# Kernel tuning notes

Measured on AMD Instinct MI355X. Metric: run time of the kernel, lower is better.

The kernel has to match this reference:

```python
import jax, jax.numpy as jnp
import numpy as np

D_MODEL = 1024
D_INNER = 2048   # expand * d_model
D_STATE = 16
D_CONV = 4
DT_RANK = 64     # ceil(d_model / 16)
BATCH = 2
SEQLEN = 4096


def setup_inputs() -> dict:
    key = jax.random.key(0)
    ks = jax.random.split(key, 9)
    g = lambda k, shape, scale: jax.random.normal(k, shape, dtype=jnp.float32) * scale
    hidden_states = g(ks[0], (BATCH, SEQLEN, D_MODEL), 1.0)
    W_in = g(ks[1], (2 * D_INNER, D_MODEL), D_MODEL ** -0.5)
    conv_w = g(ks[2], (D_INNER, D_CONV), D_CONV ** -0.5)
    conv_b = g(ks[3], (D_INNER,), 0.02)
    x_proj_w = g(ks[4], (DT_RANK + 2 * D_STATE, D_INNER), D_INNER ** -0.5)
    dt_w = g(ks[5], (D_INNER, DT_RANK), DT_RANK ** -0.5)
    # dt bias init as in Mamba: inverse softplus of dt ~ U[log(1e-3), log(1e-1)]
    dt = jnp.exp(jax.random.uniform(ks[6], (D_INNER,), dtype=jnp.float32)
                 * (np.log(0.1) - np.log(0.001)) + np.log(0.001))
    dt = jnp.clip(dt, 1e-4, None)
    dt_b = dt + jnp.log(-jnp.expm1(-dt))
    # A_log init: log of [1..d_state] repeated per channel
    A_log = jnp.log(jnp.tile(jnp.arange(1, D_STATE + 1, dtype=jnp.float32), (D_INNER, 1)))
    D = jnp.ones((D_INNER,), dtype=jnp.float32)
    W_out = g(ks[7], (D_MODEL, D_INNER), D_INNER ** -0.5)
    return dict(hidden_states=hidden_states, W_in=W_in, conv_w=conv_w, conv_b=conv_b,
                x_proj_w=x_proj_w, dt_w=dt_w, dt_b=dt_b, A_log=A_log, D=D, W_out=W_out)


def reference(hidden_states, W_in, conv_w, conv_b, x_proj_w, dt_w, dt_b, A_log, D, W_out):
    B, L, _ = hidden_states.shape
    # in_proj + transpose -> (B, 2*Din, L)
    xz = jnp.einsum('bld,ed->bel', hidden_states, W_in)
    # nanotron (tp=1) splits via view(B, d_inner, 2, L): interleaved channels
    xz = xz.reshape(B, D_INNER, 2, L)
    x, z = xz[:, :, 0, :], xz[:, :, 1, :]          # (B, Din, L)
    # causal depthwise conv1d (pad left d_conv-1) + SiLU
    xc = jax.lax.conv_general_dilated(
        x, conv_w[:, None, :], window_strides=(1,), padding=[(D_CONV - 1, 0)],
        dimension_numbers=('NCH', 'OIH', 'NCH'), feature_group_count=D_INNER)
    x = jax.nn.silu(xc + conv_b[None, :, None])     # (B, Din, L)
    # x_proj -> dt, B, C
    x_dbl = jnp.einsum('bdl,ed->ble', x, x_proj_w)  # (B, L, dt_rank+2N)
    dt, Bm, Cm = jnp.split(x_dbl, [DT_RANK, DT_RANK + D_STATE], axis=-1)
    delta = jnp.einsum('blr,dr->bdl', dt, dt_w)     # (B, Din, L)
    delta = jax.nn.softplus(delta + dt_b[None, :, None])
    A = -jnp.exp(A_log)                             # (Din, N)
    # selective scan over time
    xs = (jnp.transpose(delta, (2, 0, 1)),          # (L, B, Din)
          jnp.transpose(x, (2, 0, 1)),              # (L, B, Din)
          jnp.transpose(Bm, (1, 0, 2)),             # (L, B, N)
          jnp.transpose(Cm, (1, 0, 2)))             # (L, B, N)

    def step(s, inp):
        d_t, x_t, B_t, C_t = inp
        s = s * jnp.exp(d_t[:, :, None] * A[None]) + (d_t * x_t)[:, :, None] * B_t[:, None, :]
        y_t = jnp.einsum('bdn,bn->bd', s, C_t)
        return s, y_t

    s0 = jnp.zeros((B, D_INNER, D_STATE), dtype=hidden_states.dtype)
    _, ys = jax.lax.scan(step, s0, xs)              # ys: (L, B, Din)
    y = jnp.transpose(ys, (1, 2, 0))                # (B, Din, L)
    y = y + D[None, :, None] * x
    y = y * jax.nn.silu(z)
    out = jnp.einsum('bdl,md->blm', y, W_out)       # (B, L, d_model)
    return out
```

## Files before the change

### kernel.cpp

```cpp
#include <hip/hip_runtime.h>
#include <hip/hip_bf16.h>

#define D_MODEL 1024
#define D_INNER 2048
#define D_STATE 16
#define DT_RANK 64
#define BATCH 2
#define SEQLEN 4096
#define BL (BATCH * SEQLEN)
#define NPROJ (DT_RANK + 2 * D_STATE)
#define CH 64
#define NCH (SEQLEN / CH)

typedef __attribute__((ext_vector_type(8))) short bf16x8;
typedef __attribute__((ext_vector_type(4))) float f32x4;
struct S4 { short x, y, z, w; };

__device__ __forceinline__ float sigmoidf_(float v) {
    return 1.0f / (1.0f + __expf(-v));
}

__device__ __forceinline__ unsigned short bf16_rne(float f) {
    unsigned u = __float_as_uint(f);
    unsigned r = u + 0x7FFFu + ((u >> 16) & 1u);
    return (unsigned short)(r >> 16);
}

__device__ __forceinline__ float bf2f(short s) {
    return __uint_as_float(((unsigned)(unsigned short)s) << 16);
}

__global__ __launch_bounds__(256)
void cvt_split(const float* __restrict__ in, short* __restrict__ hi,
               short* __restrict__ lo, int n4) {
    const int i = blockIdx.x * 256 + threadIdx.x;
    if (i >= n4) return;
    const float4 v = reinterpret_cast<const float4*>(in)[i];
    const float f[4] = {v.x, v.y, v.z, v.w};
    S4 h, l;
    short hb[4], lb[4];
#pragma unroll
    for (int j = 0; j < 4; ++j) {
        const unsigned short hh = bf16_rne(f[j]);
        const float hf = __uint_as_float((unsigned)hh << 16);
        hb[j] = (short)hh;
        lb[j] = (short)bf16_rne(f[j] - hf);
    }
    h.x = hb[0]; h.y = hb[1]; h.z = hb[2]; h.w = hb[3];
    l.x = lb[0]; l.y = lb[1]; l.z = lb[2]; l.w = lb[3];
    *reinterpret_cast<S4*>(hi + (size_t)i * 4) = h;
    *reinterpret_cast<S4*>(lo + (size_t)i * 4) = l;
}

template <int EPI>
__global__ __launch_bounds__(256)
void gemm_bf16x3(const short* __restrict__ Ahi, const short* __restrict__ Alo,
                 const short* __restrict__ Bhi, const short* __restrict__ Blo,
                 float* __restrict__ C, int K, int lda, int ldb, int ldc,
                 const float* __restrict__ bias) {
    __shared__ short sA[2][128][32];
    __shared__ short sB[2][128][32];
    const int t = threadIdx.x;
    const int w = t >> 6, l = t & 63;

    const int nwg = gridDim.x * gridDim.y;
    int bid = blockIdx.y * gridDim.x + blockIdx.x;
    if ((nwg & 7) == 0) bid = (bid & 7) * (nwg >> 3) + (bid >> 3);
    const int m0 = (bid / gridDim.x) * 128, n0 = (bid % gridDim.x) * 128;
    const int wr = w >> 1, wc = w & 1;

    const short* gsrc;
    short* sdst;
    int ld, tile0;
    if (w == 0)      { gsrc = Ahi; sdst = &sA[0][0][0]; tile0 = m0; ld = lda; }
    else if (w == 1) { gsrc = Alo; sdst = &sA[1][0][0]; tile0 = m0; ld = lda; }
    else if (w == 2) { gsrc = Bhi; sdst = &sB[0][0][0]; tile0 = n0; ld = ldb; }
    else             { gsrc = Blo; sdst = &sB[1][0][0]; tile0 = n0; ld = ldb; }
    const int kc_src = ((l & 3) ^ ((l >> 3) & 3)) << 3;
    const size_t grow = (size_t)(tile0 + (l >> 2)) * ld + kc_src;

    f32x4 acc[4][4] = {};
    const int frow = l & 15;
    const int kb = (((l >> 4) ^ ((frow >> 1) & 3)) << 3);

    for (int k0 = 0; k0 < K; k0 += 32) {
        __syncthreads();
#pragma unroll
        for (int i = 0; i < 8; ++i) {
            const short* g = gsrc + grow + (size_t)(i << 4) * ld + k0;
            __builtin_amdgcn_global_load_lds(
                (const __attribute__((address_space(1))) void*)g,
                (__attribute__((address_space(3))) void*)(sdst + (i << 9)),
                16, 0, 0);
        }
        __syncthreads();

        bf16x8 a[2][4], b[2][4];
#pragma unroll
        for (int f = 0; f < 4; ++f) {
            a[0][f] = *reinterpret_cast<const bf16x8*>(&sA[0][wr * 64 + f * 16 + frow][kb]);
            a[1][f] = *reinterpret_cast<const bf16x8*>(&sA[1][wr * 64 + f * 16 + frow][kb]);
            b[0][f] = *reinterpret_cast<const bf16x8*>(&sB[0][wc * 64 + f * 16 + frow][kb]);
            b[1][f] = *reinterpret_cast<const bf16x8*>(&sB[1][wc * 64 + f * 16 + frow][kb]);
        }
#pragma unroll
        for (int fi = 0; fi < 4; ++fi)
#pragma unroll
            for (int fj = 0; fj < 4; ++fj) {
                acc[fi][fj] = __builtin_amdgcn_mfma_f32_16x16x32_bf16(
                    a[0][fi], b[0][fj], acc[fi][fj], 0, 0, 0);
                acc[fi][fj] = __builtin_amdgcn_mfma_f32_16x16x32_bf16(
                    a[1][fi], b[0][fj], acc[fi][fj], 0, 0, 0);
                acc[fi][fj] = __builtin_amdgcn_mfma_f32_16x16x32_bf16(
                    a[0][fi], b[1][fj], acc[fi][fj], 0, 0, 0);
            }
    }

    const int crow = (l >> 4) << 2;
    const int ccol = l & 15;
#pragma unroll
    for (int fi = 0; fi < 4; ++fi)
#pragma unroll
        for (int fj = 0; fj < 4; ++fj) {
            const int n = n0 + wc * 64 + fj * 16 + ccol;
#pragma unroll
            for (int r = 0; r < 4; ++r) {
                float v = acc[fi][fj][r];
                if (EPI == 1) {
                    v += bias[n];
                    v = fmaxf(v, 0.f) + log1pf(__expf(-fabsf(v)));
                }
                C[(size_t)(m0 + wr * 64 + fi * 16 + crow + r) * ldc + n] = v;
            }
        }
}

__global__ __launch_bounds__(256)
void gemm96(const short* __restrict__ Xhi, const short* __restrict__ Xlo,
            const short* __restrict__ Whi, const short* __restrict__ Wlo,
            float* __restrict__ C, short* __restrict__ dthi,
            short* __restrict__ dtlo) {
    const int t = threadIdx.x;
    const int w = t >> 6, l = t & 63;
    const int m0 = blockIdx.x * 32;
    const int rfrag = (w >> 1) * 16;
    const int cbase = (w & 1) * 48;
    const int lrow = l & 15;
    const int koff0 = (l >> 4) << 3;
    f32x4 acc[3] = {};
    const size_t arow = (size_t)(m0 + rfrag + lrow) * D_INNER;
#pragma unroll 2
    for (int k0 = 0; k0 < D_INNER; k0 += 32) {
        const int ko = k0 + koff0;
        const bf16x8 ah = *reinterpret_cast<const bf16x8*>(Xhi + arow + ko);
        const bf16x8 al = *reinterpret_cast<const bf16x8*>(Xlo + arow + ko);
#pragma unroll
        for (int jj = 0; jj < 3; ++jj) {
            const size_t brow = (size_t)(cbase + jj * 16 + lrow) * D_INNER + ko;
            const bf16x8 bh = *reinterpret_cast<const bf16x8*>(Whi + brow);
            const bf16x8 bl = *reinterpret_cast<const bf16x8*>(Wlo + brow);
            acc[jj] = __builtin_amdgcn_mfma_f32_16x16x32_bf16(ah, bh, acc[jj], 0, 0, 0);
            acc[jj] = __builtin_amdgcn_mfma_f32_16x16x32_bf16(al, bh, acc[jj], 0, 0, 0);
            acc[jj] = __builtin_amdgcn_mfma_f32_16x16x32_bf16(ah, bl, acc[jj], 0, 0, 0);
        }
    }
    const int crow = (l >> 4) << 2;
#pragma unroll
    for (int jj = 0; jj < 3; ++jj) {
        const int col = cbase + jj * 16 + lrow;
#pragma unroll
        for (int r = 0; r < 4; ++r) {
            const int m = m0 + rfrag + crow + r;
            const float v = acc[jj][r];
            C[(size_t)m * NPROJ + col] = v;
            if (col < DT_RANK) {
                const unsigned short hh = bf16_rne(v);
                dthi[(size_t)m * DT_RANK + col] = (short)hh;
                dtlo[(size_t)m * DT_RANK + col] =
                    (short)bf16_rne(v - __uint_as_float((unsigned)hh << 16));
            }
        }
    }
}

__global__ __launch_bounds__(256)
void conv_silu_k(const float* __restrict__ xr, const float* __restrict__ cw,
                 const float* __restrict__ cb, short* __restrict__ xchi,
                 short* __restrict__ xclo) {
    const int idx = blockIdx.x * 256 + threadIdx.x;
    const int d = idx & (D_INNER - 1);
    const int bl = idx >> 11;
    const int l = bl & (SEQLEN - 1);
    const float4 w4 = *reinterpret_cast<const float4*>(cw + (size_t)d * 4);
    const float wj[4] = {w4.x, w4.y, w4.z, w4.w};
    float acc = cb[d];
#pragma unroll
    for (int j = 0; j < 4; ++j) {
        const int ll = l - 3 + j;
        if (ll >= 0)
            acc += xr[(size_t)(bl - 3 + j) * D_INNER + d] * wj[j];
    }
    const float v = acc * sigmoidf_(acc);
    const unsigned short hh = bf16_rne(v);
    xchi[idx] = (short)hh;
    xclo[idx] = (short)bf16_rne(v - __uint_as_float((unsigned)hh << 16));
}

__global__ __launch_bounds__(256)
void scan1(const float* __restrict__ delta, const short* __restrict__ xchi,
           const short* __restrict__ xclo, const float* __restrict__ dtbc,
           const float* __restrict__ A_log, float* __restrict__ sum_delta,
           float* __restrict__ S_end) {
    const int d = blockIdx.x * 256 + threadIdx.x;
    const int b = blockIdx.y;
    const int c = blockIdx.z;
    __shared__ float bc[CH][32];
    for (int i = threadIdx.x; i < CH * 32; i += 256) {
        const int row = i >> 5, col = i & 31;
        bc[row][col] = dtbc[(size_t)(b * SEQLEN + c * CH + row) * NPROJ + DT_RANK + col];
    }
    __syncthreads();
    float A[16];
#pragma unroll
    for (int n = 0; n < 16; ++n) A[n] = -__expf(A_log[(size_t)d * 16 + n]);
    float s[16] = {0.f};
    float sd = 0.f;
    const size_t base = ((size_t)b * SEQLEN + (size_t)c * CH) * D_INNER + d;
    for (int li = 0; li < CH; ++li) {
        const size_t o = base + (size_t)li * D_INNER;
        const float dl = delta[o];
        const float xv = bf2f(xchi[o]) + bf2f(xclo[o]);
        sd += dl;
        const float dx = dl * xv;
#pragma unroll
        for (int n = 0; n < 16; ++n) {
            const float a = __expf(dl * A[n]);
            s[n] = fmaf(s[n], a, dx * bc[li][n]);
        }
    }
    sum_delta[((size_t)c * BATCH + b) * D_INNER + d] = sd;
#pragma unroll
    for (int n = 0; n < 16; ++n)
        S_end[(((size_t)c * BATCH + b) * 16 + n) * D_INNER + d] = s[n];
}

__global__ __launch_bounds__(256)
void scan2(const float* __restrict__ sum_delta, float* __restrict__ S,
           const float* __restrict__ A_log) {
    const int idx = blockIdx.x * 256 + threadIdx.x;
    const int d = idx & (D_INNER - 1);
    const int n = (idx >> 11) & 15;
    const int b = idx >> 15;
    const float A = -__expf(A_log[(size_t)d * 16 + n]);
    float carry = 0.f;
    for (int c = 0; c < NCH; ++c) {
        const float sd = sum_delta[((size_t)c * BATCH + b) * D_INNER + d];
        const size_t o = (((size_t)c * BATCH + b) * 16 + n) * D_INNER + d;
        const float se = S[o];
        S[o] = carry;
        carry = fmaf(carry, __expf(sd * A), se);
    }
}

__global__ __launch_bounds__(256)
void scan3(const float* __restrict__ delta, short* __restrict__ xchi,
           short* __restrict__ xclo, const float* __restrict__ z,
           const float* __restrict__ dtbc, const float* __restrict__ A_log,
           const float* __restrict__ S_init, const float* __restrict__ Dp) {
    const int d = blockIdx.x * 256 + threadIdx.x;
    const int b = blockIdx.y;
    const int c = blockIdx.z;
    __shared__ float bc[CH][32];
    for (int i = threadIdx.x; i < CH * 32; i += 256) {
        const int row = i >> 5, col = i & 31;
        bc[row][col] = dtbc[(size_t)(b * SEQLEN + c * CH + row) * NPROJ + DT_RANK + col];
    }
    __syncthreads();
    float A[16];
#pragma unroll
    for (int n = 0; n < 16; ++n) A[n] = -__expf(A_log[(size_t)d * 16 + n]);
    float s[16];
#pragma unroll
    for (int n = 0; n < 16; ++n)
        s[n] = S_init[(((size_t)c * BATCH + b) * 16 + n) * D_INNER + d];
    const float Dv = Dp[d];
    const size_t base = ((size_t)b * SEQLEN + (size_t)c * CH) * D_INNER + d;
    for (int li = 0; li < CH; ++li) {
        const size_t o = base + (size_t)li * D_INNER;
        const float dl = delta[o];
        const float xv = bf2f(xchi[o]) + bf2f(xclo[o]);
        const float dx = dl * xv;
        float y = 0.f;
#pragma unroll
        for (int n = 0; n < 16; ++n) {
            const float a = __expf(dl * A[n]);
            s[n] = fmaf(s[n], a, dx * bc[li][n]);
            y = fmaf(s[n], bc[li][16 + n], y);
        }
        const float zv = z[o];
        const float yv = (y + Dv * xv) * (zv * sigmoidf_(zv));
        const unsigned short hh = bf16_rne(yv);
        xchi[o] = (short)hh;
        xclo[o] = (short)bf16_rne(yv - __uint_as_float((unsigned)hh << 16));
    }
}

extern "C" void kernel_launch(void* const* d_in, const int* in_sizes, int n_in,
                              void* d_out, int out_size, void* d_ws, size_t ws_size,
                              hipStream_t stream) {
    const float* hidden   = (const float*)d_in[0];
    const float* W_in     = (const float*)d_in[1];
    const float* conv_w   = (const float*)d_in[2];
    const float* conv_b   = (const float*)d_in[3];
    const float* x_proj_w = (const float*)d_in[4];
    const float* dt_w     = (const float*)d_in[5];
    const float* dt_b     = (const float*)d_in[6];
    const float* A_log    = (const float*)d_in[7];
    const float* Dp       = (const float*)d_in[8];
    const float* W_out    = (const float*)d_in[9];
    float* out = (float*)d_out;

    float* ws    = (float*)d_ws;
    float* xbuf  = ws;
    float* zbuf  = xbuf + (size_t)BL * D_INNER;
    float* xcreg = zbuf + (size_t)BL * D_INNER;
    float* dtbc  = xcreg + (size_t)BL * D_INNER;
    float* sumd  = dtbc + (size_t)BL * NPROJ;
    float* Send  = sumd + (size_t)NCH * BATCH * D_INNER;

    short* xpwhi = (short*)(Send + (size_t)NCH * BATCH * 16 * D_INNER);
    short* xpwlo = xpwhi + (size_t)NPROJ * D_INNER;
    short* dtwhi = xpwlo + (size_t)NPROJ * D_INNER;
    short* dtwlo = dtwhi + (size_t)D_INNER * DT_RANK;
    short* dthi  = dtwlo + (size_t)D_INNER * DT_RANK;
    short* dtlo  = dthi + (size_t)BL * DT_RANK;

    short* hxhi  = (short*)xcreg;
    short* hxlo  = hxhi + (size_t)BL * D_MODEL;
    short* winhi = hxlo + (size_t)BL * D_MODEL;
    short* winlo = winhi + (size_t)2 * D_INNER * D_MODEL;

    const dim3 thr(256);

    cvt_split<<<dim3(BL * D_MODEL / 1024), thr, 0, stream>>>(hidden, hxhi, hxlo, BL * D_MODEL / 4);
    cvt_split<<<dim3(2 * D_INNER * D_MODEL / 1024), thr, 0, stream>>>(W_in, winhi, winlo, 2 * D_INNER * D_MODEL / 4);
    cvt_split<<<dim3(NPROJ * D_INNER / 1024), thr, 0, stream>>>(x_proj_w, xpwhi, xpwlo, NPROJ * D_INNER / 4);
    cvt_split<<<dim3(D_INNER * DT_RANK / 1024), thr, 0, stream>>>(dt_w, dtwhi, dtwlo, D_INNER * DT_RANK / 4);

    gemm_bf16x3<0><<<dim3(D_INNER / 128, BL / 128), thr, 0, stream>>>(
        hxhi, hxlo, winhi, winlo, xbuf, D_MODEL, D_MODEL, 2 * D_MODEL, D_INNER, nullptr);
    gemm_bf16x3<0><<<dim3(D_INNER / 128, BL / 128), thr, 0, stream>>>(
        hxhi, hxlo, winhi + D_MODEL, winlo + D_MODEL, zbuf, D_MODEL, D_MODEL, 2 * D_MODEL, D_INNER, nullptr);

    short* xchi = (short*)xcreg;
    short* xclo = xchi + (size_t)BL * D_INNER;
    conv_silu_k<<<dim3(BL * D_INNER / 256), thr, 0, stream>>>(xbuf, conv_w, conv_b, xchi, xclo);

    gemm96<<<dim3(BL / 32), thr, 0, stream>>>(xchi, xclo, xpwhi, xpwlo, dtbc, dthi, dtlo);

    gemm_bf16x3<1><<<dim3(D_INNER / 128, BL / 128), thr, 0, stream>>>(
        dthi, dtlo, dtwhi, dtwlo, xbuf, DT_RANK, DT_RANK, DT_RANK, D_INNER, dt_b);

    scan1<<<dim3(D_INNER / 256, BATCH, NCH), thr, 0, stream>>>(
        xbuf, xchi, xclo, dtbc, A_log, sumd, Send);
    scan2<<<dim3(BATCH * 16 * D_INNER / 256), thr, 0, stream>>>(sumd, Send, A_log);
    scan3<<<dim3(D_INNER / 256, BATCH, NCH), thr, 0, stream>>>(
        xbuf, xchi, xclo, zbuf, dtbc, A_log, Send, Dp);

    short* wohi = (short*)zbuf;
    short* wolo = wohi + (size_t)D_MODEL * D_INNER;
    cvt_split<<<dim3(D_MODEL * D_INNER / 1024), thr, 0, stream>>>(W_out, wohi, wolo, D_MODEL * D_INNER / 4);

    gemm_bf16x3<0><<<dim3(D_MODEL / 128, BL / 128), thr, 0, stream>>>(
        xchi, xclo, wohi, wolo, out, D_INNER, D_INNER, D_INNER, D_MODEL, nullptr);
}
```

Before: 762.9 us.

## Double-buffer LDS tiles in bf16x3 GEMM to overlap global loads with MFMA

Doubles the shared-memory tiles and restructures the K loop so the next K-slice is fetched with global_load_lds while MFMAs run on the current slice. Explicit vmcnt waits and s_barrier calls replace the two __syncthreads per iteration. This hides global-to-LDS latency in the GEMMs, at the cost of twice the LDS per block (64KB), which may lower occupancy.

```diff
diff --git a/kernel.cpp b/kernel.cpp
--- a/kernel.cpp
+++ b/kernel.cpp
@@ -58,8 +58,8 @@
                  const short* __restrict__ Bhi, const short* __restrict__ Blo,
                  float* __restrict__ C, int K, int lda, int ldb, int ldc,
                  const float* __restrict__ bias) {
-    __shared__ short sA[2][128][32];
-    __shared__ short sB[2][128][32];
+    __shared__ short sA[2][2][128][32];
+    __shared__ short sB[2][2][128][32];
     const int t = threadIdx.x;
     const int w = t >> 6, l = t & 63;
 
@@ -70,12 +70,13 @@
     const int wr = w >> 1, wc = w & 1;
 
     const short* gsrc;
-    short* sdst;
+    short* sd0;
+    short* sd1;
     int ld, tile0;
-    if (w == 0)      { gsrc = Ahi; sdst = &sA[0][0][0]; tile0 = m0; ld = lda; }
-    else if (w == 1) { gsrc = Alo; sdst = &sA[1][0][0]; tile0 = m0; ld = lda; }
-    else if (w == 2) { gsrc = Bhi; sdst = &sB[0][0][0]; tile0 = n0; ld = ldb; }
-    else             { gsrc = Blo; sdst = &sB[1][0][0]; tile0 = n0; ld = ldb; }
+    if (w == 0)      { gsrc = Ahi; sd0 = &sA[0][0][0][0]; sd1 = &sA[1][0][0][0]; tile0 = m0; ld = lda; }
+    else if (w == 1) { gsrc = Alo; sd0 = &sA[0][1][0][0]; sd1 = &sA[1][1][0][0]; tile0 = m0; ld = lda; }
+    else if (w == 2) { gsrc = Bhi; sd0 = &sB[0][0][0][0]; sd1 = &sB[1][0][0][0]; tile0 = n0; ld = ldb; }
+    else             { gsrc = Blo; sd0 = &sB[0][1][0][0]; sd1 = &sB[1][1][0][0]; tile0 = n0; ld = ldb; }
     const int kc_src = ((l & 3) ^ ((l >> 3) & 3)) << 3;
     const size_t grow = (size_t)(tile0 + (l >> 2)) * ld + kc_src;
 
@@ -83,8 +84,7 @@
     const int frow = l & 15;
     const int kb = (((l >> 4) ^ ((frow >> 1) & 3)) << 3);
 
-    for (int k0 = 0; k0 < K; k0 += 32) {
-        __syncthreads();
+    auto STAGE = [&](short* sdst, int k0) {
 #pragma unroll
         for (int i = 0; i < 8; ++i) {
             const short* g = gsrc + grow + (size_t)(i << 4) * ld + k0;
@@ -93,15 +93,16 @@
                 (__attribute__((address_space(3))) void*)(sdst + (i << 9)),
                 16, 0, 0);
         }
-        __syncthreads();
-
+    };
+
+    auto COMPUTE = [&](int cur) {
         bf16x8 a[2][4], b[2][4];
 #pragma unroll
         for (int f = 0; f < 4; ++f) {
-            a[0][f] = *reinterpret_cast<const bf16x8*>(&sA[0][wr * 64 + f * 16 + frow][kb]);
-            a[1][f] = *reinterpret_cast<const bf16x8*>(&sA[1][wr * 64 + f * 16 + frow][kb]);
-            b[0][f] = *reinterpret_cast<const bf16x8*>(&sB[0][wc * 64 + f * 16 + frow][kb]);
-            b[1][f] = *reinterpret_cast<const bf16x8*>(&sB[1][wc * 64 + f * 16 + frow][kb]);
+            a[0][f] = *reinterpret_cast<const bf16x8*>(&sA[cur][0][wr * 64 + f * 16 + frow][kb]);
+            a[1][f] = *reinterpret_cast<const bf16x8*>(&sA[cur][1][wr * 64 + f * 16 + frow][kb]);
+            b[0][f] = *reinterpret_cast<const bf16x8*>(&sB[cur][0][wc * 64 + f * 16 + frow][kb]);
+            b[1][f] = *reinterpret_cast<const bf16x8*>(&sB[cur][1][wc * 64 + f * 16 + frow][kb]);
         }
 #pragma unroll
         for (int fi = 0; fi < 4; ++fi)
@@ -114,6 +115,26 @@
                 acc[fi][fj] = __builtin_amdgcn_mfma_f32_16x16x32_bf16(
                     a[0][fi], b[1][fj], acc[fi][fj], 0, 0, 0);
             }
+    };
+
+    const int NT = K >> 5;
+    STAGE(sd0, 0);
+    for (int tt = 0; tt < NT - 1; ++tt) {
+        const int cur = tt & 1;
+        STAGE(cur ? sd0 : sd1, (tt + 1) << 5);
+        __builtin_amdgcn_sched_barrier(0);
+        asm volatile("s_waitcnt vmcnt(8)" ::: "memory");
+        __builtin_amdgcn_s_barrier();
+        COMPUTE(cur);
+        __builtin_amdgcn_sched_barrier(0);
+        __builtin_amdgcn_s_barrier();
+    }
+    {
+        const int cur = (NT - 1) & 1;
+        __builtin_amdgcn_sched_barrier(0);
+        asm volatile("s_waitcnt vmcnt(0)" ::: "memory");
+        __builtin_amdgcn_s_barrier();
+        COMPUTE(cur);
     }
 
     const int crow = (l >> 4) << 2;
```

Result: faster. 709.4 us (-7.0%).

## Switch split GEMMs to fp16 two-term MFMA with fused x/z pipelined GEMM

Applied to the files above, without the earlier changes.

The three-term bf16 split (hi*hi + lo*hi + hi*lo) is replaced by an fp16 two-term split: only the activation keeps a hi/lo pair and the weight is a single fp16 value. The aim is to cut the MFMA count and the weight conversion and load traffic. The GEMM kernel moves to 256x128 tiles with 512 threads and a triple-buffered global_load_lds pipeline using explicit vmcnt waits. The x and z in_proj GEMMs are fused into one launch that splits the interleaved output columns in the epilogue. Delta and z are now stored as fp16 to halve scan traffic, at some risk to accuracy and fp16 range.

```diff
diff --git a/kernel.cpp b/kernel.cpp
--- a/kernel.cpp
+++ b/kernel.cpp
@@ -12,27 +12,39 @@
 #define CH 64
 #define NCH (SEQLEN / CH)
 
-typedef __attribute__((ext_vector_type(8))) short bf16x8;
+typedef __attribute__((ext_vector_type(8))) _Float16 f16x8;
 typedef __attribute__((ext_vector_type(4))) float f32x4;
 struct S4 { short x, y, z, w; };
 
 __device__ __forceinline__ float sigmoidf_(float v) {
     return 1.0f / (1.0f + __expf(-v));
 }
-
-__device__ __forceinline__ unsigned short bf16_rne(float f) {
-    unsigned u = __float_as_uint(f);
-    unsigned r = u + 0x7FFFu + ((u >> 16) & 1u);
-    return (unsigned short)(r >> 16);
-}
-
-__device__ __forceinline__ float bf2f(short s) {
-    return __uint_as_float(((unsigned)(unsigned short)s) << 16);
-}
-
-__global__ __launch_bounds__(256)
-void cvt_split(const float* __restrict__ in, short* __restrict__ hi,
-               short* __restrict__ lo, int n4) {
+__device__ __forceinline__ short f2h(float f) {
+    _Float16 h = (_Float16)f;
+    return __builtin_bit_cast(short, h);
+}
+__device__ __forceinline__ float h2f(short s) {
+    return (float)__builtin_bit_cast(_Float16, s);
+}
+
+#define GLOAD(gptr, dptr)                                              \
+    __builtin_amdgcn_global_load_lds(                                  \
+        (const __attribute__((address_space(1))) void*)(gptr),         \
+        (__attribute__((address_space(3))) void*)(dptr), 16, 0, 0)
+
+__global__ __launch_bounds__(256)
+void cvt_h(const float* __restrict__ in, short* __restrict__ out, int n4) {
+    const int i = blockIdx.x * 256 + threadIdx.x;
+    if (i >= n4) return;
+    const float4 v = reinterpret_cast<const float4*>(in)[i];
+    S4 o;
+    o.x = f2h(v.x); o.y = f2h(v.y); o.z = f2h(v.z); o.w = f2h(v.w);
+    *reinterpret_cast<S4*>(out + (size_t)i * 4) = o;
+}
+
+__global__ __launch_bounds__(256)
+void cvt_split_h(const float* __restrict__ in, short* __restrict__ hi,
+                 short* __restrict__ lo, int n4) {
     const int i = blockIdx.x * 256 + threadIdx.x;
     if (i >= n4) return;
     const float4 v = reinterpret_cast<const float4*>(in)[i];
@@ -41,10 +53,8 @@
     short hb[4], lb[4];
 #pragma unroll
     for (int j = 0; j < 4; ++j) {
-        const unsigned short hh = bf16_rne(f[j]);
-        const float hf = __uint_as_float((unsigned)hh << 16);
-        hb[j] = (short)hh;
-        lb[j] = (short)bf16_rne(f[j] - hf);
+        hb[j] = f2h(f[j]);
+        lb[j] = f2h(f[j] - h2f(hb[j]));
     }
     h.x = hb[0]; h.y = hb[1]; h.z = hb[2]; h.w = hb[3];
     l.x = lb[0]; l.y = lb[1]; l.z = lb[2]; l.w = lb[3];
@@ -53,67 +63,75 @@
 }
 
 template <int EPI>
-__global__ __launch_bounds__(256)
-void gemm_bf16x3(const short* __restrict__ Ahi, const short* __restrict__ Alo,
-                 const short* __restrict__ Bhi, const short* __restrict__ Blo,
-                 float* __restrict__ C, int K, int lda, int ldb, int ldc,
-                 const float* __restrict__ bias) {
-    __shared__ short sA[2][128][32];
-    __shared__ short sB[2][128][32];
+__global__ __launch_bounds__(512)
+void gemm_f16x2(const short* __restrict__ Ahi, const short* __restrict__ Alo,
+                const short* __restrict__ B, void* C0v, void* C1v,
+                int K, int lda, int ldb, int ldc,
+                const float* __restrict__ bias) {
+    extern __shared__ short smem[];
     const int t = threadIdx.x;
     const int w = t >> 6, l = t & 63;
 
     const int nwg = gridDim.x * gridDim.y;
     int bid = blockIdx.y * gridDim.x + blockIdx.x;
-    if ((nwg & 7) == 0) bid = (bid & 7) * (nwg >> 3) + (bid >> 3);
-    const int m0 = (bid / gridDim.x) * 128, n0 = (bid % gridDim.x) * 128;
+    bid = (bid & 7) * (nwg >> 3) + (bid >> 3);
+    const int m0 = (bid / gridDim.x) * 256, n0 = (bid % gridDim.x) * 128;
     const int wr = w >> 1, wc = w & 1;
 
-    const short* gsrc;
-    short* sdst;
-    int ld, tile0;
-    if (w == 0)      { gsrc = Ahi; sdst = &sA[0][0][0]; tile0 = m0; ld = lda; }
-    else if (w == 1) { gsrc = Alo; sdst = &sA[1][0][0]; tile0 = m0; ld = lda; }
-    else if (w == 2) { gsrc = Bhi; sdst = &sB[0][0][0]; tile0 = n0; ld = ldb; }
-    else             { gsrc = Blo; sdst = &sB[1][0][0]; tile0 = n0; ld = ldb; }
+    const int r4 = l >> 2;
     const int kc_src = ((l & 3) ^ ((l >> 3) & 3)) << 3;
-    const size_t grow = (size_t)(tile0 + (l >> 2)) * ld + kc_src;
-
-    f32x4 acc[4][4] = {};
     const int frow = l & 15;
     const int kb = (((l >> 4) ^ ((frow >> 1) & 3)) << 3);
 
-    for (int k0 = 0; k0 < K; k0 += 32) {
-        __syncthreads();
-#pragma unroll
-        for (int i = 0; i < 8; ++i) {
-            const short* g = gsrc + grow + (size_t)(i << 4) * ld + k0;
-            __builtin_amdgcn_global_load_lds(
-                (const __attribute__((address_space(1))) void*)g,
-                (__attribute__((address_space(3))) void*)(sdst + (i << 9)),
-                16, 0, 0);
-        }
-        __syncthreads();
-
-        bf16x8 a[2][4], b[2][4];
+    f32x4 acc[4][4] = {};
+
+    auto STAGE = [&](int buf, int k0) {
+        short* bb = smem + buf * 20480;
+        const int s0 = 2 * w, s1 = 2 * w + 1;
+        GLOAD(Ahi + (size_t)(m0 + s0 * 16 + r4) * lda + k0 + kc_src, bb + s0 * 512);
+        GLOAD(Ahi + (size_t)(m0 + s1 * 16 + r4) * lda + k0 + kc_src, bb + s1 * 512);
+        GLOAD(Alo + (size_t)(m0 + s0 * 16 + r4) * lda + k0 + kc_src, bb + 8192 + s0 * 512);
+        GLOAD(Alo + (size_t)(m0 + s1 * 16 + r4) * lda + k0 + kc_src, bb + 8192 + s1 * 512);
+        GLOAD(B + (size_t)(n0 + w * 16 + r4) * ldb + k0 + kc_src, bb + 16384 + w * 512);
+    };
+
+    auto COMPUTE = [&](int buf) {
+        const short* bb = smem + buf * 20480;
+        f16x8 ah[4], al[4], bv[4];
 #pragma unroll
         for (int f = 0; f < 4; ++f) {
-            a[0][f] = *reinterpret_cast<const bf16x8*>(&sA[0][wr * 64 + f * 16 + frow][kb]);
-            a[1][f] = *reinterpret_cast<const bf16x8*>(&sA[1][wr * 64 + f * 16 + frow][kb]);
-            b[0][f] = *reinterpret_cast<const bf16x8*>(&sB[0][wc * 64 + f * 16 + frow][kb]);
-            b[1][f] = *reinterpret_cast<const bf16x8*>(&sB[1][wc * 64 + f * 16 + frow][kb]);
+            ah[f] = *reinterpret_cast<const f16x8*>(&bb[(wr * 64 + f * 16 + frow) * 32 + kb]);
+            al[f] = *reinterpret_cast<const f16x8*>(&bb[8192 + (wr * 64 + f * 16 + frow) * 32 + kb]);
+            bv[f] = *reinterpret_cast<const f16x8*>(&bb[16384 + (wc * 64 + f * 16 + frow) * 32 + kb]);
         }
 #pragma unroll
         for (int fi = 0; fi < 4; ++fi)
 #pragma unroll
             for (int fj = 0; fj < 4; ++fj) {
-                acc[fi][fj] = __builtin_amdgcn_mfma_f32_16x16x32_bf16(
-                    a[0][fi], b[0][fj], acc[fi][fj], 0, 0, 0);
-                acc[fi][fj] = __builtin_amdgcn_mfma_f32_16x16x32_bf16(
-                    a[1][fi], b[0][fj], acc[fi][fj], 0, 0, 0);
-                acc[fi][fj] = __builtin_amdgcn_mfma_f32_16x16x32_bf16(
-                    a[0][fi], b[1][fj], acc[fi][fj], 0, 0, 0);
+                acc[fi][fj] = __builtin_amdgcn_mfma_f32_16x16x32_f16(
+                    ah[fi], bv[fj], acc[fi][fj], 0, 0, 0);
+                acc[fi][fj] = __builtin_amdgcn_mfma_f32_16x16x32_f16(
+                    al[fi], bv[fj], acc[fi][fj], 0, 0, 0);
             }
+    };
+
+    const int NT = K >> 5;
+    STAGE(0, 0);
+    STAGE(1, 32);
+    for (int tt = 0; tt < NT; ++tt) {
+        const int cur = tt % 3;
+        if (tt + 2 < NT) STAGE((tt + 2) % 3, (tt + 2) << 5);
+        __builtin_amdgcn_sched_barrier(0);
+        if (tt < NT - 2)
+            asm volatile("s_waitcnt vmcnt(10)" ::: "memory");
+        else if (tt == NT - 2)
+            asm volatile("s_waitcnt vmcnt(5)" ::: "memory");
+        else
+            asm volatile("s_waitcnt vmcnt(0)" ::: "memory");
+        __builtin_amdgcn_s_barrier();
+        COMPUTE(cur);
+        __builtin_amdgcn_sched_barrier(0);
+        __builtin_amdgcn_s_barrier();
     }
 
     const int crow = (l >> 4) << 2;
@@ -125,21 +143,26 @@
             const int n = n0 + wc * 64 + fj * 16 + ccol;
 #pragma unroll
             for (int r = 0; r < 4; ++r) {
-                float v = acc[fi][fj][r];
-                if (EPI == 1) {
-                    v += bias[n];
-                    v = fmaxf(v, 0.f) + log1pf(__expf(-fabsf(v)));
+                const float v = acc[fi][fj][r];
+                const size_t row = (size_t)(m0 + wr * 64 + fi * 16 + crow + r);
+                if (EPI == 0) {
+                    ((float*)C0v)[row * ldc + n] = v;
+                } else if (EPI == 1) {
+                    float s = v + bias[n];
+                    s = fmaxf(s, 0.f) + log1pf(__expf(-fabsf(s)));
+                    ((short*)C0v)[row * ldc + n] = f2h(s);
+                } else {
+                    if (n & 1) ((short*)C1v)[row * ldc + (n >> 1)] = f2h(v);
+                    else       ((float*)C0v)[row * ldc + (n >> 1)] = v;
                 }
-                C[(size_t)(m0 + wr * 64 + fi * 16 + crow + r) * ldc + n] = v;
             }
         }
 }
 
 __global__ __launch_bounds__(256)
 void gemm96(const short* __restrict__ Xhi, const short* __restrict__ Xlo,
-            const short* __restrict__ Whi, const short* __restrict__ Wlo,
-            float* __restrict__ C, short* __restrict__ dthi,
-            short* __restrict__ dtlo) {
+            const short* __restrict__ W, float* __restrict__ C,
+            short* __restrict__ dthi, short* __restrict__ dtlo) {
     const int t = threadIdx.x;
     const int w = t >> 6, l = t & 63;
     const int m0 = blockIdx.x * 32;
@@ -152,16 +175,14 @@
 #pragma unroll 2
     for (int k0 = 0; k0 < D_INNER; k0 += 32) {
         const int ko = k0 + koff0;
-        const bf16x8 ah = *reinterpret_cast<const bf16x8*>(Xhi + arow + ko);
-        const bf16x8 al = *reinterpret_cast<const bf16x8*>(Xlo + arow + ko);
+        const f16x8 ah = *reinterpret_cast<const f16x8*>(Xhi + arow + ko);
+        const f16x8 al = *reinterpret_cast<const f16x8*>(Xlo + arow + ko);
 #pragma unroll
         for (int jj = 0; jj < 3; ++jj) {
             const size_t brow = (size_t)(cbase + jj * 16 + lrow) * D_INNER + ko;
-            const bf16x8 bh = *reinterpret_cast<const bf16x8*>(Whi + brow);
-            const bf16x8 bl = *reinterpret_cast<const bf16x8*>(Wlo + brow);
-            acc[jj] = __builtin_amdgcn_mfma_f32_16x16x32_bf16(ah, bh, acc[jj], 0, 0, 0);
-            acc[jj] = __builtin_amdgcn_mfma_f32_16x16x32_bf16(al, bh, acc[jj], 0, 0, 0);
-            acc[jj] = __builtin_amdgcn_mfma_f32_16x16x32_bf16(ah, bl, acc[jj], 0, 0, 0);
+            const f16x8 bw = *reinterpret_cast<const f16x8*>(W + brow);
+            acc[jj] = __builtin_amdgcn_mfma_f32_16x16x32_f16(ah, bw, acc[jj], 0, 0, 0);
+            acc[jj] = __builtin_amdgcn_mfma_f32_16x16x32_f16(al, bw, acc[jj], 0, 0, 0);
         }
     }
     const int crow = (l >> 4) << 2;
@@ -174,10 +195,9 @@
             const float v = acc[jj][r];
             C[(size_t)m * NPROJ + col] = v;
             if (col < DT_RANK) {
-                const unsigned short hh = bf16_rne(v);
-                dthi[(size_t)m * DT_RANK + col] = (short)hh;
-                dtlo[(size_t)m * DT_RANK + col] =
-                    (short)bf16_rne(v - __uint_as_float((unsigned)hh << 16));
+                const short hh = f2h(v);
+                dthi[(size_t)m * DT_RANK + col] = hh;
+                dtlo[(size_t)m * DT_RANK + col] = f2h(v - h2f(hh));
             }
         }
     }
@@ -201,13 +221,13 @@
             acc += xr[(size_t)(bl - 3 + j) * D_INNER + d] * wj[j];
     }
     const float v = acc * sigmoidf_(acc);
-    const unsigned short hh = bf16_rne(v);
-    xchi[idx] = (short)hh;
-    xclo[idx] = (short)bf16_rne(v - __uint_as_float((unsigned)hh << 16));
-}
-
-__global__ __launch_bounds__(256)
-void scan1(const float* __restrict__ delta, const short* __restrict__ xchi,
+    const short hh = f2h(v);
+    xchi[idx] = hh;
+    xclo[idx] = f2h(v - h2f(hh));
+}
+
+__global__ __launch_bounds__(256)
+void scan1(const short* __restrict__ delta, const short* __restrict__ xchi,
            const short* __restrict__ xclo, const float* __restrict__ dtbc,
            const float* __restrict__ A_log, float* __restrict__ sum_delta,
            float* __restrict__ S_end) {
@@ -228,8 +248,8 @@
     const size_t base = ((size_t)b * SEQLEN + (size_t)c * CH) * D_INNER + d;
     for (int li = 0; li < CH; ++li) {
         const size_t o = base + (size_t)li * D_INNER;
-        const float dl = delta[o];
-        const float xv = bf2f(xchi[o]) + bf2f(xclo[o]);
+        const float dl = h2f(delta[o]);
+        const float xv = h2f(xchi[o]) + h2f(xclo[o]);
         sd += dl;
         const float dx = dl * xv;
 #pragma unroll
@@ -263,8 +283,8 @@
 }
 
 __global__ __launch_bounds__(256)
-void scan3(const float* __restrict__ delta, short* __restrict__ xchi,
-           short* __restrict__ xclo, const float* __restrict__ z,
+void scan3(const short* __restrict__ delta, short* __restrict__ xchi,
+           short* __restrict__ xclo, const short* __restrict__ z,
            const float* __restrict__ dtbc, const float* __restrict__ A_log,
            const float* __restrict__ S_init, const float* __restrict__ Dp) {
     const int d = blockIdx.x * 256 + threadIdx.x;
@@ -287,8 +307,8 @@
     const size_t base = ((size_t)b * SEQLEN + (size_t)c * CH) * D_INNER + d;
     for (int li = 0; li < CH; ++li) {
         const size_t o = base + (size_t)li * D_INNER;
-        const float dl = delta[o];
-        const float xv = bf2f(xchi[o]) + bf2f(xclo[o]);
+        const float dl = h2f(delta[o]);
+        const float xv = h2f(xchi[o]) + h2f(xclo[o]);
         const float dx = dl * xv;
         float y = 0.f;
 #pragma unroll
@@ -297,11 +317,11 @@
             s[n] = fmaf(s[n], a, dx * bc[li][n]);
             y = fmaf(s[n], bc[li][16 + n], y);
         }
-        const float zv = z[o];
+        const float zv = h2f(z[o]);
         const float yv = (y + Dv * xv) * (zv * sigmoidf_(zv));
-        const unsigned short hh = bf16_rne(yv);
-        xchi[o] = (short)hh;
-        xclo[o] = (short)bf16_rne(yv - __uint_as_float((unsigned)hh << 16));
+        const short hh = f2h(yv);
+        xchi[o] = hh;
+        xclo[o] = f2h(yv - h2f(hh));
     }
 }
 
@@ -328,49 +348,45 @@
     float* sumd  = dtbc + (size_t)BL * NPROJ;
     float* Send  = sumd + (size_t)NCH * BATCH * D_INNER;
 
-    short* xpwhi = (short*)(Send + (size_t)NCH * BATCH * 16 * D_INNER);
-    short* xpwlo = xpwhi + (size_t)NPROJ * D_INNER;
-    short* dtwhi = xpwlo + (size_t)NPROJ * D_INNER;
-    short* dtwlo = dtwhi + (size_t)D_INNER * DT_RANK;
-    short* dthi  = dtwlo + (size_t)D_INNER * DT_RANK;
-    short* dtlo  = dthi + (size_t)BL * DT_RANK;
-
-    short* hxhi  = (short*)xcreg;
-    short* hxlo  = hxhi + (size_t)BL * D_MODEL;
-    short* winhi = hxlo + (size_t)BL * D_MODEL;
-    short* winlo = winhi + (size_t)2 * D_INNER * D_MODEL;
+    short* xpwh = (short*)(Send + (size_t)NCH * BATCH * 16 * D_INNER);
+    short* dtwh = xpwh + (size_t)NPROJ * D_INNER;
+    short* dthi = dtwh + (size_t)D_INNER * DT_RANK;
+    short* dtlo = dthi + (size_t)BL * DT_RANK;
+
+    short* hxhi = (short*)xcreg;
+    short* hxlo = hxhi + (size_t)BL * D_MODEL;
+    short* winh = hxlo + (size_t)BL * D_MODEL;
 
     const dim3 thr(256);
 
-    cvt_split<<<dim3(BL * D_MODEL / 1024), thr, 0, stream>>>(hidden, hxhi, hxlo, BL * D_MODEL / 4);
-    cvt_split<<<dim3(2 * D_INNER * D_MODEL / 1024), thr, 0, stream>>>(W_in, winhi, winlo, 2 * D_INNER * D_MODEL / 4);
-    cvt_split<<<dim3(NPROJ * D_INNER / 1024), thr, 0, stream>>>(x_proj_w, xpwhi, xpwlo, NPROJ * D_INNER / 4);
-    cvt_split<<<dim3(D_INNER * DT_RANK / 1024), thr, 0, stream>>>(dt_w, dtwhi, dtwlo, D_INNER * DT_RANK / 4);
-
-    gemm_bf16x3<0><<<dim3(D_INNER / 128, BL / 128), thr, 0, stream>>>(
-        hxhi, hxlo, winhi, winlo, xbuf, D_MODEL, D_MODEL, 2 * D_MODEL, D_INNER, nullptr);
-    gemm_bf16x3<0><<<dim3(D_INNER / 128, BL / 128), thr, 0, stream>>>(
-        hxhi, hxlo, winhi + D_MODEL, winlo + D_MODEL, zbuf, D_MODEL, D_MODEL, 2 * D_MODEL, D_INNER, nullptr);
+    cvt_split_h<<<dim3(BL * D_MODEL / 1024), thr, 0, stream>>>(hidden, hxhi, hxlo, BL * D_MODEL / 4);
+    cvt_h<<<dim3(2 * D_INNER * D_MODEL / 1024), thr, 0, stream>>>(W_in, winh, 2 * D_INNER * D_MODEL / 4);
+    cvt_h<<<dim3(NPROJ * D_INNER / 1024), thr, 0, stream>>>(x_proj_w, xpwh, NPROJ * D_INNER / 4);
+    cvt_h<<<dim3(D_INNER * DT_RANK / 1024), thr, 0, stream>>>(dt_w, dtwh, D_INNER * DT_RANK / 4);
+
+    short* zh = (short*)zbuf;
+    gemm_f16x2<2><<<dim3(2 * D_INNER / 128, BL / 256), dim3(512), 122880, stream>>>(
+        hxhi, hxlo, winh, xbuf, zh, D_MODEL, D_MODEL, D_MODEL, D_INNER, nullptr);
 
     short* xchi = (short*)xcreg;
     short* xclo = xchi + (size_t)BL * D_INNER;
     conv_silu_k<<<dim3(BL * D_INNER / 256), thr, 0, stream>>>(xbuf, conv_w, conv_b, xchi, xclo);
 
-    gemm96<<<dim3(BL / 32), thr, 0, stream>>>(xchi, xclo, xpwhi, xpwlo, dtbc, dthi, dtlo);
-
-    gemm_bf16x3<1><<<dim3(D_INNER / 128, BL / 128), thr, 0, stream>>>(
-        dthi, dtlo, dtwhi, dtwlo, xbuf, DT_RANK, DT_RANK, DT_RANK, D_INNER, dt_b);
+    gemm96<<<dim3(BL / 32), thr, 0, stream>>>(xchi, xclo, xpwh, dtbc, dthi, dtlo);
+
+    short* deltah = (short*)xbuf;
+    gemm_f16x2<1><<<dim3(D_INNER / 128, BL / 256), dim3(512), 122880, stream>>>(
+        dthi, dtlo, dtwh, deltah, nullptr, DT_RANK, DT_RANK, DT_RANK, D_INNER, dt_b);
 
     scan1<<<dim3(D_INNER / 256, BATCH, NCH), thr, 0, stream>>>(
-        xbuf, xchi, xclo, dtbc, A_log, sumd, Send);
+        deltah, xchi, xclo, dtbc, A_log, sumd, Send);
     scan2<<<dim3(BATCH * 16 * D_INNER / 256), thr, 0, stream>>>(sumd, Send, A_log);
     scan3<<<dim3(D_INNER / 256, BATCH, NCH), thr, 0, stream>>>(
-        xbuf, xchi, xclo, zbuf, dtbc, A_log, Send, Dp);
-
-    short* wohi = (short*)zbuf;
-    short* wolo = wohi + (size_t)D_MODEL * D_INNER;
-    cvt_split<<<dim3(D_MODEL * D_INNER / 1024), thr, 0, stream>>>(W_out, wohi, wolo, D_MODEL * D_INNER / 4);
-
-    gemm_bf16x3<0><<<dim3(D_MODEL / 128, BL / 128), thr, 0, stream>>>(
-        xchi, xclo, wohi, wolo, out, D_INNER, D_INNER, D_INNER, D_MODEL, nullptr);
-}
+        deltah, xchi, xclo, zh, dtbc, A_log, Send, Dp);
+
+    short* woh = (short*)zbuf;
+    cvt_h<<<dim3(D_MODEL * D_INNER / 1024), thr, 0, stream>>>(W_out, woh, D_MODEL * D_INNER / 4);
+
+    gemm_f16x2<0><<<dim3(D_MODEL / 128, BL / 256), dim3(512), 122880, stream>>>(
+        xchi, xclo, woh, out, nullptr, D_INNER, D_INNER, D_INNER, D_MODEL, nullptr);
+}
```

Result: faster. 658.5 us (-13.7%).
